# Optimization experiments

Hardware: AMD Instinct MI355X
Metric: run time of the kernel (lower is better)

Reference implementation:

```python
import jax, jax.numpy as jnp
import numpy as np

# Dims: R radiance slots (patch,direction), E sparse transfer entries, T echogram samples, P patches
R, E, T, P = 4096, 131072, 1536, 256
NUM_BOUNCES = 12
FSM_GAMMA = 1e-3
SAMPLE_RATE = 16000.0


def setup_inputs() -> dict:
    key = jax.random.key(0)
    ks = jax.random.split(key, 10)
    initial_radiance = jax.random.normal(ks[0], (R, T), dtype=jnp.float32)
    # basis scaled so per-bounce operator row-sums < 1 (stable recursion, as real kernels are)
    basis = jax.random.uniform(ks[1], (2, E), dtype=jnp.float32) * (1.0 / 64.0)
    absorption = jax.random.uniform(ks[2], (P,), dtype=jnp.float32)
    scattering = jax.random.uniform(ks[3], (P,), dtype=jnp.float32)
    detection_weights = jax.random.uniform(ks[4], (R,), dtype=jnp.float32)
    row = jax.random.randint(ks[5], (E,), 0, R)
    col = jax.random.randint(ks[6], (E,), 0, R)
    reflector_ids = jax.random.randint(ks[7], (E,), 0, P)
    delay_samples = jax.random.randint(ks[8], (E,), 0, 512)
    detection_delay = jax.random.randint(ks[9], (R,), 0, 256)
    return dict(initial_radiance=initial_radiance, basis=basis, absorption=absorption,
                scattering=scattering, detection_weights=detection_weights,
                row=row, col=col, reflector_ids=reflector_ids,
                delay_samples=delay_samples, detection_delay=detection_delay)


def reference(initial_radiance, basis, absorption, scattering, detection_weights,
              row, col, reflector_ids, delay_samples, detection_delay):
    Rn, Tn = initial_radiance.shape
    F = Tn // 2 + 1
    # FSM damping window exp(log(gamma) * t), undone after the frequency-domain loop
    t = jnp.arange(Tn, dtype=jnp.float32) / SAMPLE_RATE
    fsm_window = jnp.exp(np.float32(np.log(FSM_GAMMA)) * t)  # [T]
    # compose_kernel: per-edge reflection kernel from per-patch absorption/scattering
    a = absorption[reflector_ids]
    s = scattering[reflector_ids]
    kern = (1.0 - a) * (s * basis[0] + (1.0 - s) * basis[1])  # [E]
    # per-edge integer-delay as frequency-domain phase ramp
    f = jnp.arange(F, dtype=jnp.float32)
    edge_phase = jnp.exp(-2j * np.pi * (delay_samples.astype(jnp.float32)[:, None] * f[None, :] / Tn))
    kc = kern.astype(jnp.complex64)[:, None] * edge_phase.astype(jnp.complex64)  # [E, F]
    # injected radiance in frequency domain (damped)
    Xf = jnp.fft.rfft(initial_radiance * fsm_window[None, :], axis=-1).astype(jnp.complex64)  # [R, F]

    def bounce(carry, _):
        cur, tot = carry
        msg = kc * cur[col]                                    # gather + sparse multiply [E, F]
        nxt = jax.ops.segment_sum(msg, row, num_segments=Rn)   # scatter-add -> [R, F]
        return (nxt, tot + nxt), None

    (_, total), _ = jax.lax.scan(bounce, (Xf, Xf), None, length=NUM_BOUNCES)
    # detection: per-radiance delayed weighted sum at the receiver
    det_phase = jnp.exp(-2j * np.pi * (detection_delay.astype(jnp.float32)[:, None] * f[None, :] / Tn))
    echo_f = jnp.einsum('r,rf->f', detection_weights.astype(jnp.complex64),
                        det_phase.astype(jnp.complex64) * total)
    echogram = jnp.fft.irfft(echo_f, n=Tn) / fsm_window  # FSM correction
    return echogram
```

## Files before the change

kernel.cpp:

```cpp
#include <hip/hip_runtime.h>
#include <hip/hip_bf16.h>
#include <hip/hip_fp16.h>

#define RN 4096
#define EN 131072
#define TN 1536
#define T2 768
#define SP 1040
#define PADP 257
#define PN 256
#define NBOUNCE 12
#define NCHUNK 4
#define CP 192
#define LOG_GAMMA -6.90775528f
#define INV_SR (1.0f / 16000.0f)

#define rfl(x) __builtin_amdgcn_readfirstlane(x)


__global__ void hist_kernel(const int* __restrict__ row, const int* __restrict__ col,
                            int* __restrict__ cnt2) {
    int e = blockIdx.x * blockDim.x + threadIdx.x;
    if (e < EN) atomicAdd(&cnt2[row[e] * 2 + (col[e] >> 11)], 1);
}

__global__ void scan_kernel(const int* __restrict__ cnt2, int* __restrict__ off,
                            int* __restrict__ cursor2, int* __restrict__ ntot) {
    __shared__ int part[1024];
    int tid = threadIdx.x;
    int l0 = cnt2[(tid * 4 + 0) * 2], h0 = cnt2[(tid * 4 + 0) * 2 + 1];
    int l1 = cnt2[(tid * 4 + 1) * 2], h1 = cnt2[(tid * 4 + 1) * 2 + 1];
    int l2 = cnt2[(tid * 4 + 2) * 2], h2 = cnt2[(tid * 4 + 2) * 2 + 1];
    int l3 = cnt2[(tid * 4 + 3) * 2], h3 = cnt2[(tid * 4 + 3) * 2 + 1];
    int n0 = l0 + h0, n1 = l1 + h1, n2 = l2 + h2, n3 = l3 + h3;
    int p0 = (n0 + 1) & ~1, p1 = (n1 + 1) & ~1, p2 = (n2 + 1) & ~1, p3 = (n3 + 1) & ~1;
    part[tid] = p0 + p1 + p2 + p3;
    __syncthreads();
    for (int ofs = 1; ofs < 1024; ofs <<= 1) {
        int x = (tid >= ofs) ? part[tid - ofs] : 0;
        __syncthreads();
        part[tid] += x;
        __syncthreads();
    }
    int excl = (tid == 0) ? 0 : part[tid - 1];
    int o0 = excl, o1 = o0 + p0, o2 = o1 + p1, o3 = o2 + p2;
    int r0 = tid * 4;
    off[r0 + 0] = o0; cursor2[(r0 + 0) * 2] = o0; cursor2[(r0 + 0) * 2 + 1] = o0 + l0; ntot[r0 + 0] = n0;
    off[r0 + 1] = o1; cursor2[(r0 + 1) * 2] = o1; cursor2[(r0 + 1) * 2 + 1] = o1 + l1; ntot[r0 + 1] = n1;
    off[r0 + 2] = o2; cursor2[(r0 + 2) * 2] = o2; cursor2[(r0 + 2) * 2 + 1] = o2 + l2; ntot[r0 + 2] = n2;
    off[r0 + 3] = o3; cursor2[(r0 + 3) * 2] = o3; cursor2[(r0 + 3) * 2 + 1] = o3 + l3; ntot[r0 + 3] = n3;
    if (tid == 1023) off[RN] = o3 + p3;
}

__global__ void scatter_kernel(const int* __restrict__ row, const int* __restrict__ col,
                               const int* __restrict__ rid, const int* __restrict__ delay,
                               const float* __restrict__ basis,
                               const float* __restrict__ absorption,
                               const float* __restrict__ scattering,
                               int* __restrict__ cursor2, int2* __restrict__ mdarr) {
    int e = blockIdx.x * blockDim.x + threadIdx.x;
    if (e >= EN) return;
    int p = rid[e];
    float a = absorption[p];
    float s = scattering[p];
    float k = (1.0f - a) * (s * basis[e] + (1.0f - s) * basis[EN + e]);
    int d = delay[e];
    int c = col[e];
    int dpair = (d + 1) >> 1;
    int o = ((c * SP + PADP - dpair) << 2) | (d & 1);
    int pos = atomicAdd(&cursor2[row[e] * 2 + (c >> 11)], 1);
    mdarr[pos] = make_int2(o, __float_as_int(k));
}

__global__ void padfill_kernel(const int* __restrict__ off, const int* __restrict__ ntot,
                               int2* __restrict__ mdarr) {
    int r = blockIdx.x * 256 + threadIdx.x;
    if (r < RN) {
        int n = ntot[r];
        if (n & 1) mdarr[off[r] + n] = make_int2(PADP << 2, 0);
    }
    if (r < 8) mdarr[off[RN] + r] = make_int2(PADP << 2, 0);
}


__global__ __launch_bounds__(256) void init_kernel(const float* __restrict__ x,
                                                   __half* __restrict__ cur) {
    int r = blockIdx.x;
    int tid = threadIdx.x;
    const float* xr = x + r * TN;
    uint* curp = (uint*)cur + (size_t)r * SP;
#pragma unroll
    for (int kk = 0; kk < 3; ++kk) {
        int q = tid + kk * 256;
        int t = q * 2;
        float wa = __expf(LOG_GAMMA * (float)t * INV_SR);
        float wb = __expf(LOG_GAMMA * (float)(t + 1) * INV_SR);
        __half2 h = __float22half2_rn(make_float2(xr[t] * wa, xr[t + 1] * wb));
        uint u = *(uint*)&h;
        curp[PADP + q] = u;
        if (q >= 511) curp[q - 511] = u;
    }
}


#define ISSUE(W, mo)                                                   \
    {                                                                  \
        const uint* rp_ = (const uint*)(curb + (size_t)((mo) & ~1u));  \
        W = *(const uint4*)(rp_ + pb);                                 \
    }

#define CONSUME(W, mo, kb)                                             \
    {                                                                  \
        float k_ = __uint_as_float((uint)(kb));                        \
        uint v0_, v1_, v2_;                                            \
        if ((mo) & 1u) {                                               \
            v0_ = __builtin_amdgcn_alignbit(W.y, W.x, 16);             \
            v1_ = __builtin_amdgcn_alignbit(W.z, W.y, 16);             \
            v2_ = __builtin_amdgcn_alignbit(W.w, W.z, 16);             \
        } else { v0_ = W.x; v1_ = W.y; v2_ = W.z; }                    \
        __half2 h0_ = *(__half2*)&v0_;                                 \
        __half2 h1_ = *(__half2*)&v1_;                                 \
        __half2 h2_ = *(__half2*)&v2_;                                 \
        a0 = fmaf(k_, __half2float(h0_.x), a0);                        \
        a1 = fmaf(k_, __half2float(h0_.y), a1);                        \
        a2 = fmaf(k_, __half2float(h1_.x), a2);                        \
        a3 = fmaf(k_, __half2float(h1_.y), a3);                        \
        a4 = fmaf(k_, __half2float(h2_.x), a4);                        \
        a5 = fmaf(k_, __half2float(h2_.y), a5);                        \
    }

__global__ __launch_bounds__(128, 8) void bounce_kernel(
        const __half* __restrict__ cur, __half* __restrict__ nxt,
        const int* __restrict__ offp, const int* __restrict__ ntot,
        const int2* __restrict__ mdarr) {
    int bid = blockIdx.x;
    int rg = bid >> 2;
    int chunk = bid & 3;
    int wave = threadIdx.x >> 6;
    int lane = threadIdx.x & 63;
    int r = rg * 2 + wave;
    int c0 = chunk * CP;
    int pb = c0 + lane * 3;
    int e0 = rfl(offp[r]);
    int n  = rfl(ntot[r]);
    float a0 = 0.f, a1 = 0.f, a2 = 0.f, a3 = 0.f, a4 = 0.f, a5 = 0.f;
    const char* curb = (const char*)cur;

    if (n > 0) {
        int e1p = e0 + ((n + 1) & ~1);
        uint4 md01 = *(const uint4*)(mdarr + e0);
        uint moA = (uint)rfl((int)md01.x), kbA = (uint)rfl((int)md01.y);
        uint moB = (uint)rfl((int)md01.z), kbB = (uint)rfl((int)md01.w);
        uint4 WA, WB;
        ISSUE(WA, moA);
        ISSUE(WB, moB);
        for (int j = e0 + 2; j < e1p; j += 2) {
            uint4 mdn = *(const uint4*)(mdarr + j);
            uint moC = (uint)rfl((int)mdn.x), kbC = (uint)rfl((int)mdn.y);
            uint moD = (uint)rfl((int)mdn.z), kbD = (uint)rfl((int)mdn.w);
            CONSUME(WA, moA, kbA); ISSUE(WA, moC);
            CONSUME(WB, moB, kbB); ISSUE(WB, moD);
            moA = moC; kbA = kbC; moB = moD; kbB = kbD;
        }
        CONSUME(WA, moA, kbA);
        CONSUME(WB, moB, kbB);
    }

    __half2 h0 = __float22half2_rn(make_float2(a0, a1));
    __half2 h1 = __float22half2_rn(make_float2(a2, a3));
    __half2 h2 = __float22half2_rn(make_float2(a4, a5));
    uint u0 = *(uint*)&h0, u1 = *(uint*)&h1, u2 = *(uint*)&h2;
    uint* nxtp = (uint*)nxt + (size_t)r * SP;
    nxtp[PADP + pb]     = u0;
    nxtp[PADP + pb + 1] = u1;
    nxtp[PADP + pb + 2] = u2;
    if (pb + 2 >= 511) {
        if (pb     >= 511) nxtp[pb - 511] = u0;
        if (pb + 1 >= 511) nxtp[pb - 510] = u1;
        nxtp[pb - 509] = u2;
    }
}


__global__ __launch_bounds__(128) void detect_kernel(
        const __half* __restrict__ buf, const float* __restrict__ w,
        const int* __restrict__ dd, float* __restrict__ det) {
    int cx = blockIdx.x;
    int r0 = blockIdx.y * 16;
    int tid = threadIdx.x;
    int tb = cx * 384 + tid;
    float acc0 = 0.f, acc1 = 0.f, acc2 = 0.f;
#pragma unroll 4
    for (int rr = 0; rr < 16; ++rr) {
        int r = r0 + rr;
        int d = dd[r];
        float wr = w[r];
        const __half* bufr = buf + (size_t)r * (SP * 2);
        int s0 = tb - d;           if (s0 < 0) s0 += TN;
        int s1 = tb + 128 - d;     if (s1 < 0) s1 += TN;
        int s2 = tb + 256 - d;     if (s2 < 0) s2 += TN;
        acc0 = fmaf(wr, __half2float(bufr[(PADP + (s0 >> 1)) * 2 + (s0 & 1)]), acc0);
        acc1 = fmaf(wr, __half2float(bufr[(PADP + (s1 >> 1)) * 2 + (s1 & 1)]), acc1);
        acc2 = fmaf(wr, __half2float(bufr[(PADP + (s2 >> 1)) * 2 + (s2 & 1)]), acc2);
    }
    atomicAdd(&det[tb], acc0);
    atomicAdd(&det[tb + 128], acc1);
    atomicAdd(&det[tb + 256], acc2);
}

__global__ void final_kernel(const float* __restrict__ det, float* __restrict__ out) {
    int t = blockIdx.x * 256 + threadIdx.x;
    if (t < TN) out[t] = det[t] * __expf(-LOG_GAMMA * (float)t * INV_SR);
}


extern "C" void kernel_launch(void* const* d_in, const int* in_sizes, int n_in,
                              void* d_out, int out_size, void* d_ws, size_t ws_size,
                              hipStream_t stream) {
    const float* init_rad   = (const float*)d_in[0];
    const float* basis      = (const float*)d_in[1];
    const float* absorption = (const float*)d_in[2];
    const float* scattering = (const float*)d_in[3];
    const float* det_w      = (const float*)d_in[4];
    const int*   row        = (const int*)d_in[5];
    const int*   col        = (const int*)d_in[6];
    const int*   rid        = (const int*)d_in[7];
    const int*   delay      = (const int*)d_in[8];
    const int*   det_delay  = (const int*)d_in[9];
    float* out = (float*)d_out;

    char* ws = (char*)d_ws;
    size_t o = 0;
    auto alloc = [&](size_t bytes) {
        void* p = ws + o;
        o = (o + bytes + 255) & ~(size_t)255;
        return p;
    };
    int*    cnt2    = (int*)alloc(RN * 2 * 4);
    int*    off     = (int*)alloc((RN + 1) * 4);
    int*    cursor2 = (int*)alloc(RN * 2 * 4);
    int*    ntot    = (int*)alloc(RN * 4);
    int2*   mdarr   = (int2*)alloc((size_t)(EN + RN + 8) * 8);
    __half* bufA    = (__half*)alloc((size_t)RN * SP * 4);
    __half* bufB    = (__half*)alloc((size_t)RN * SP * 4);
    float*  det     = (float*)alloc(TN * 4);

    hipMemsetAsync(cnt2, 0, RN * 2 * 4, stream);
    hipMemsetAsync(det, 0, TN * 4, stream);

    hist_kernel<<<EN / 256, 256, 0, stream>>>(row, col, cnt2);
    scan_kernel<<<1, 1024, 0, stream>>>(cnt2, off, cursor2, ntot);
    scatter_kernel<<<EN / 256, 256, 0, stream>>>(row, col, rid, delay, basis,
                                                 absorption, scattering, cursor2, mdarr);
    padfill_kernel<<<RN / 256, 256, 0, stream>>>(off, ntot, mdarr);
    init_kernel<<<RN, 256, 0, stream>>>(init_rad, bufA);

    dim3 dgrid(NCHUNK, RN / 16);
    detect_kernel<<<dgrid, 128, 0, stream>>>(bufA, det_w, det_delay, det);

    __half* cur = bufA;
    __half* nxt = bufB;
    for (int b = 0; b < NBOUNCE; ++b) {
        bounce_kernel<<<(RN / 2) * NCHUNK, 128, 0, stream>>>(cur, nxt, off, ntot, mdarr);
        detect_kernel<<<dgrid, 128, 0, stream>>>(nxt, det_w, det_delay, det);
        __half* tmp = cur; cur = nxt; nxt = tmp;
    }

    final_kernel<<<TN / 256, 256, 0, stream>>>(det, out);
}
```

Measured before the change: 627.4 us.

## Process four rows per wave in low/high column phases for gather locality

Each bounce wave now handles four rows spread across the matrix and sweeps all their low-column edges before the high-column edges, so gathers hit the same half of the source buffer together and cache reuse should improve. Separate low/high counters replace the interleaved histogram, and the even-padding of edge lists plus the padfill kernel are removed. The edge loop becomes a one-deep prefetch pipeline, occupancy hints drop to 4 blocks, and output stores become nontemporal. The trade is less memory-level parallelism per wave and more registers in exchange for locality.

```diff
diff --git a/kernel.cpp b/kernel.cpp
--- a/kernel.cpp
+++ b/kernel.cpp
@@ -19,22 +19,25 @@
 
 
 __global__ void hist_kernel(const int* __restrict__ row, const int* __restrict__ col,
-                            int* __restrict__ cnt2) {
+                            int* __restrict__ cntL, int* __restrict__ cntH) {
     int e = blockIdx.x * blockDim.x + threadIdx.x;
-    if (e < EN) atomicAdd(&cnt2[row[e] * 2 + (col[e] >> 11)], 1);
-}
-
-__global__ void scan_kernel(const int* __restrict__ cnt2, int* __restrict__ off,
-                            int* __restrict__ cursor2, int* __restrict__ ntot) {
+    if (e >= EN) return;
+    int r = row[e];
+    if (col[e] < 2048) atomicAdd(&cntL[r], 1);
+    else               atomicAdd(&cntH[r], 1);
+}
+
+__global__ void scan_kernel(const int* __restrict__ cntL, const int* __restrict__ cntH,
+                            int* __restrict__ off, int* __restrict__ curL,
+                            int* __restrict__ curH) {
     __shared__ int part[1024];
     int tid = threadIdx.x;
-    int l0 = cnt2[(tid * 4 + 0) * 2], h0 = cnt2[(tid * 4 + 0) * 2 + 1];
-    int l1 = cnt2[(tid * 4 + 1) * 2], h1 = cnt2[(tid * 4 + 1) * 2 + 1];
-    int l2 = cnt2[(tid * 4 + 2) * 2], h2 = cnt2[(tid * 4 + 2) * 2 + 1];
-    int l3 = cnt2[(tid * 4 + 3) * 2], h3 = cnt2[(tid * 4 + 3) * 2 + 1];
+    int l0 = cntL[tid * 4 + 0], h0 = cntH[tid * 4 + 0];
+    int l1 = cntL[tid * 4 + 1], h1 = cntH[tid * 4 + 1];
+    int l2 = cntL[tid * 4 + 2], h2 = cntH[tid * 4 + 2];
+    int l3 = cntL[tid * 4 + 3], h3 = cntH[tid * 4 + 3];
     int n0 = l0 + h0, n1 = l1 + h1, n2 = l2 + h2, n3 = l3 + h3;
-    int p0 = (n0 + 1) & ~1, p1 = (n1 + 1) & ~1, p2 = (n2 + 1) & ~1, p3 = (n3 + 1) & ~1;
-    part[tid] = p0 + p1 + p2 + p3;
+    part[tid] = n0 + n1 + n2 + n3;
     __syncthreads();
     for (int ofs = 1; ofs < 1024; ofs <<= 1) {
         int x = (tid >= ofs) ? part[tid - ofs] : 0;
@@ -43,13 +46,13 @@
         __syncthreads();
     }
     int excl = (tid == 0) ? 0 : part[tid - 1];
-    int o0 = excl, o1 = o0 + p0, o2 = o1 + p1, o3 = o2 + p2;
+    int o0 = excl, o1 = o0 + n0, o2 = o1 + n1, o3 = o2 + n2;
     int r0 = tid * 4;
-    off[r0 + 0] = o0; cursor2[(r0 + 0) * 2] = o0; cursor2[(r0 + 0) * 2 + 1] = o0 + l0; ntot[r0 + 0] = n0;
-    off[r0 + 1] = o1; cursor2[(r0 + 1) * 2] = o1; cursor2[(r0 + 1) * 2 + 1] = o1 + l1; ntot[r0 + 1] = n1;
-    off[r0 + 2] = o2; cursor2[(r0 + 2) * 2] = o2; cursor2[(r0 + 2) * 2 + 1] = o2 + l2; ntot[r0 + 2] = n2;
-    off[r0 + 3] = o3; cursor2[(r0 + 3) * 2] = o3; cursor2[(r0 + 3) * 2 + 1] = o3 + l3; ntot[r0 + 3] = n3;
-    if (tid == 1023) off[RN] = o3 + p3;
+    off[r0 + 0] = o0; curL[r0 + 0] = o0; curH[r0 + 0] = o0 + l0;
+    off[r0 + 1] = o1; curL[r0 + 1] = o1; curH[r0 + 1] = o1 + l1;
+    off[r0 + 2] = o2; curL[r0 + 2] = o2; curH[r0 + 2] = o2 + l2;
+    off[r0 + 3] = o3; curL[r0 + 3] = o3; curH[r0 + 3] = o3 + l3;
+    if (tid == 1023) off[RN] = o3 + n3;
 }
 
 __global__ void scatter_kernel(const int* __restrict__ row, const int* __restrict__ col,
@@ -57,7 +60,8 @@
                                const float* __restrict__ basis,
                                const float* __restrict__ absorption,
                                const float* __restrict__ scattering,
-                               int* __restrict__ cursor2, int2* __restrict__ mdarr) {
+                               int* __restrict__ curL, int* __restrict__ curH,
+                               int2* __restrict__ mdarr) {
     int e = blockIdx.x * blockDim.x + threadIdx.x;
     if (e >= EN) return;
     int p = rid[e];
@@ -68,18 +72,9 @@
     int c = col[e];
     int dpair = (d + 1) >> 1;
     int o = ((c * SP + PADP - dpair) << 2) | (d & 1);
-    int pos = atomicAdd(&cursor2[row[e] * 2 + (c >> 11)], 1);
+    int r = row[e];
+    int pos = (c < 2048) ? atomicAdd(&curL[r], 1) : atomicAdd(&curH[r], 1);
     mdarr[pos] = make_int2(o, __float_as_int(k));
-}
-
-__global__ void padfill_kernel(const int* __restrict__ off, const int* __restrict__ ntot,
-                               int2* __restrict__ mdarr) {
-    int r = blockIdx.x * 256 + threadIdx.x;
-    if (r < RN) {
-        int n = ntot[r];
-        if (n & 1) mdarr[off[r] + n] = make_int2(PADP << 2, 0);
-    }
-    if (r < 8) mdarr[off[RN] + r] = make_int2(PADP << 2, 0);
 }
 
 
@@ -109,7 +104,7 @@
         W = *(const uint4*)(rp_ + pb);                                 \
     }
 
-#define CONSUME(W, mo, kb)                                             \
+#define CONSUME(W, mo, kb, ACC)                                        \
     {                                                                  \
         float k_ = __uint_as_float((uint)(kb));                        \
         uint v0_, v1_, v2_;                                            \
@@ -121,63 +116,74 @@
         __half2 h0_ = *(__half2*)&v0_;                                 \
         __half2 h1_ = *(__half2*)&v1_;                                 \
         __half2 h2_ = *(__half2*)&v2_;                                 \
-        a0 = fmaf(k_, __half2float(h0_.x), a0);                        \
-        a1 = fmaf(k_, __half2float(h0_.y), a1);                        \
-        a2 = fmaf(k_, __half2float(h1_.x), a2);                        \
-        a3 = fmaf(k_, __half2float(h1_.y), a3);                        \
-        a4 = fmaf(k_, __half2float(h2_.x), a4);                        \
-        a5 = fmaf(k_, __half2float(h2_.y), a5);                        \
-    }
-
-__global__ __launch_bounds__(128, 8) void bounce_kernel(
+        ACC[0] = fmaf(k_, __half2float(h0_.x), ACC[0]);                \
+        ACC[1] = fmaf(k_, __half2float(h0_.y), ACC[1]);                \
+        ACC[2] = fmaf(k_, __half2float(h1_.x), ACC[2]);                \
+        ACC[3] = fmaf(k_, __half2float(h1_.y), ACC[3]);                \
+        ACC[4] = fmaf(k_, __half2float(h2_.x), ACC[4]);                \
+        ACC[5] = fmaf(k_, __half2float(h2_.y), ACC[5]);                \
+    }
+
+#define SEGMENT(S0, S1, ACC)                                           \
+    if ((S1) > (S0)) {                                                 \
+        int2 md = mdarr[S0];                                           \
+        uint mo = (uint)rfl(md.x), kb = (uint)rfl(md.y);               \
+        uint4 W; ISSUE(W, mo);                                         \
+        for (int j = (S0) + 1; j < (S1); ++j) {                        \
+            int2 mdn = mdarr[j];                                       \
+            uint moN = (uint)rfl(mdn.x), kbN = (uint)rfl(mdn.y);       \
+            uint4 WN; ISSUE(WN, moN);                                  \
+            CONSUME(W, mo, kb, ACC);                                   \
+            W = WN; mo = moN; kb = kbN;                                \
+        }                                                              \
+        CONSUME(W, mo, kb, ACC);                                       \
+    }
+
+__global__ __launch_bounds__(128, 4) void bounce_kernel(
         const __half* __restrict__ cur, __half* __restrict__ nxt,
-        const int* __restrict__ offp, const int* __restrict__ ntot,
+        const int* __restrict__ offp, const int* __restrict__ cntL,
         const int2* __restrict__ mdarr) {
     int bid = blockIdx.x;
-    int rg = bid >> 2;
     int chunk = bid & 3;
+    int rgrp = bid >> 2;
     int wave = threadIdx.x >> 6;
     int lane = threadIdx.x & 63;
-    int r = rg * 2 + wave;
     int c0 = chunk * CP;
     int pb = c0 + lane * 3;
-    int e0 = rfl(offp[r]);
-    int n  = rfl(ntot[r]);
-    float a0 = 0.f, a1 = 0.f, a2 = 0.f, a3 = 0.f, a4 = 0.f, a5 = 0.f;
     const char* curb = (const char*)cur;
 
-    if (n > 0) {
-        int e1p = e0 + ((n + 1) & ~1);
-        uint4 md01 = *(const uint4*)(mdarr + e0);
-        uint moA = (uint)rfl((int)md01.x), kbA = (uint)rfl((int)md01.y);
-        uint moB = (uint)rfl((int)md01.z), kbB = (uint)rfl((int)md01.w);
-        uint4 WA, WB;
-        ISSUE(WA, moA);
-        ISSUE(WB, moB);
-        for (int j = e0 + 2; j < e1p; j += 2) {
-            uint4 mdn = *(const uint4*)(mdarr + j);
-            uint moC = (uint)rfl((int)mdn.x), kbC = (uint)rfl((int)mdn.y);
-            uint moD = (uint)rfl((int)mdn.z), kbD = (uint)rfl((int)mdn.w);
-            CONSUME(WA, moA, kbA); ISSUE(WA, moC);
-            CONSUME(WB, moB, kbB); ISSUE(WB, moD);
-            moA = moC; kbA = kbC; moB = moD; kbB = kbD;
+    float acc[4][6] = {};
+
+#pragma unroll
+    for (int ph = 0; ph < 2; ++ph) {
+#pragma unroll
+        for (int L = 0; L < 4; ++L) {
+            int r = rgrp * 2 + wave + 1024 * L;
+            int o0 = rfl(offp[r]);
+            int o1 = rfl(offp[r + 1]);
+            int lo = rfl(cntL[r]);
+            int s0 = ph ? (o0 + lo) : o0;
+            int s1 = ph ? o1 : (o0 + lo);
+            SEGMENT(s0, s1, acc[L]);
         }
-        CONSUME(WA, moA, kbA);
-        CONSUME(WB, moB, kbB);
-    }
-
-    __half2 h0 = __float22half2_rn(make_float2(a0, a1));
-    __half2 h1 = __float22half2_rn(make_float2(a2, a3));
-    __half2 h2 = __float22half2_rn(make_float2(a4, a5));
-    uint u0 = *(uint*)&h0, u1 = *(uint*)&h1, u2 = *(uint*)&h2;
-    uint* nxtp = (uint*)nxt + (size_t)r * SP;
-    nxtp[PADP + pb]     = u0;
-    nxtp[PADP + pb + 1] = u1;
-    nxtp[PADP + pb + 2] = u2;
-    if (pb + 2 >= 511) {
-        if (pb     >= 511) nxtp[pb - 511] = u0;
-        if (pb + 1 >= 511) nxtp[pb - 510] = u1;
-        nxtp[pb - 509] = u2;
+    }
+
+#pragma unroll
+    for (int L = 0; L < 4; ++L) {
+        int r = rgrp * 2 + wave + 1024 * L;
+        __half2 h0 = __float22half2_rn(make_float2(acc[L][0], acc[L][1]));
+        __half2 h1 = __float22half2_rn(make_float2(acc[L][2], acc[L][3]));
+        __half2 h2 = __float22half2_rn(make_float2(acc[L][4], acc[L][5]));
+        uint u0 = *(uint*)&h0, u1 = *(uint*)&h1, u2 = *(uint*)&h2;
+        uint* nxtp = (uint*)nxt + (size_t)r * SP;
+        __builtin_nontemporal_store(u0, nxtp + PADP + pb);
+        __builtin_nontemporal_store(u1, nxtp + PADP + pb + 1);
+        __builtin_nontemporal_store(u2, nxtp + PADP + pb + 2);
+        if (pb + 2 >= 511) {
+            if (pb     >= 511) __builtin_nontemporal_store(u0, nxtp + pb - 511);
+            if (pb + 1 >= 511) __builtin_nontemporal_store(u1, nxtp + pb - 510);
+            __builtin_nontemporal_store(u2, nxtp + pb - 509);
+        }
     }
 }
 
@@ -236,23 +242,25 @@
         o = (o + bytes + 255) & ~(size_t)255;
         return p;
     };
-    int*    cnt2    = (int*)alloc(RN * 2 * 4);
-    int*    off     = (int*)alloc((RN + 1) * 4);
-    int*    cursor2 = (int*)alloc(RN * 2 * 4);
-    int*    ntot    = (int*)alloc(RN * 4);
-    int2*   mdarr   = (int2*)alloc((size_t)(EN + RN + 8) * 8);
-    __half* bufA    = (__half*)alloc((size_t)RN * SP * 4);
-    __half* bufB    = (__half*)alloc((size_t)RN * SP * 4);
-    float*  det     = (float*)alloc(TN * 4);
-
-    hipMemsetAsync(cnt2, 0, RN * 2 * 4, stream);
+    int*    cntL   = (int*)alloc(RN * 4);
+    int*    cntH   = (int*)alloc(RN * 4);
+    int*    curL   = (int*)alloc(RN * 4);
+    int*    curH   = (int*)alloc(RN * 4);
+    int*    off    = (int*)alloc((RN + 1) * 4);
+    int2*   mdarr  = (int2*)alloc((size_t)EN * 8);
+    __half* bufA   = (__half*)alloc((size_t)RN * SP * 4);
+    __half* bufB   = (__half*)alloc((size_t)RN * SP * 4);
+    float*  det    = (float*)alloc(TN * 4);
+
+    hipMemsetAsync(cntL, 0, RN * 4, stream);
+    hipMemsetAsync(cntH, 0, RN * 4, stream);
     hipMemsetAsync(det, 0, TN * 4, stream);
 
-    hist_kernel<<<EN / 256, 256, 0, stream>>>(row, col, cnt2);
-    scan_kernel<<<1, 1024, 0, stream>>>(cnt2, off, cursor2, ntot);
+    hist_kernel<<<EN / 256, 256, 0, stream>>>(row, col, cntL, cntH);
+    scan_kernel<<<1, 1024, 0, stream>>>(cntL, cntH, off, curL, curH);
     scatter_kernel<<<EN / 256, 256, 0, stream>>>(row, col, rid, delay, basis,
-                                                 absorption, scattering, cursor2, mdarr);
-    padfill_kernel<<<RN / 256, 256, 0, stream>>>(off, ntot, mdarr);
+                                                 absorption, scattering, curL, curH,
+                                                 mdarr);
     init_kernel<<<RN, 256, 0, stream>>>(init_rad, bufA);
 
     dim3 dgrid(NCHUNK, RN / 16);
@@ -261,7 +269,7 @@
     __half* cur = bufA;
     __half* nxt = bufB;
     for (int b = 0; b < NBOUNCE; ++b) {
-        bounce_kernel<<<(RN / 2) * NCHUNK, 128, 0, stream>>>(cur, nxt, off, ntot, mdarr);
+        bounce_kernel<<<2048, 128, 0, stream>>>(cur, nxt, off, cntL, mdarr);
         detect_kernel<<<dgrid, 128, 0, stream>>>(nxt, det_w, det_delay, det);
         __half* tmp = cur; cur = nxt; nxt = tmp;
     }
```

Result: slower. 941.4 us (+50.1%).

## Store radiance buffers as fp8 with byte-granular delay gathers

Applied to the files above, without the earlier changes.

The radiance state moves from fp16 pairs to fp8 (e4m3) bytes, halving the gather traffic in the bounce kernel and in detection. Edge offsets become plain byte offsets with a byte alignment shift, and output rows are repacked through LDS for aligned 8-byte stores. The initial detection pass now reads the fp32 input directly so the injected term keeps full precision. The risk is a large accuracy loss, since fp8 carries only 3 mantissa bits and a narrow range across 12 compounding bounces, and the output may fail tolerance.

```diff
diff --git a/kernel.cpp b/kernel.cpp
--- a/kernel.cpp
+++ b/kernel.cpp
@@ -5,17 +5,18 @@
 #define RN 4096
 #define EN 131072
 #define TN 1536
-#define T2 768
-#define SP 1040
-#define PADP 257
+#define SPB 2064
+#define PADB 512
 #define PN 256
 #define NBOUNCE 12
 #define NCHUNK 4
-#define CP 192
+#define CPB 384
 #define LOG_GAMMA -6.90775528f
 #define INV_SR (1.0f / 16000.0f)
 
 #define rfl(x) __builtin_amdgcn_readfirstlane(x)
+typedef float v2f __attribute__((ext_vector_type(2)));
+typedef unsigned char uchar;
 
 
 __global__ void hist_kernel(const int* __restrict__ row, const int* __restrict__ col,
@@ -64,10 +65,8 @@
     float a = absorption[p];
     float s = scattering[p];
     float k = (1.0f - a) * (s * basis[e] + (1.0f - s) * basis[EN + e]);
-    int d = delay[e];
     int c = col[e];
-    int dpair = (d + 1) >> 1;
-    int o = ((c * SP + PADP - dpair) << 2) | (d & 1);
+    int o = c * SPB + PADB - delay[e];
     int pos = atomicAdd(&cursor2[row[e] * 2 + (c >> 11)], 1);
     mdarr[pos] = make_int2(o, __float_as_int(k));
 }
@@ -77,60 +76,60 @@
     int r = blockIdx.x * 256 + threadIdx.x;
     if (r < RN) {
         int n = ntot[r];
-        if (n & 1) mdarr[off[r] + n] = make_int2(PADP << 2, 0);
-    }
-    if (r < 8) mdarr[off[RN] + r] = make_int2(PADP << 2, 0);
-}
-
-
-__global__ __launch_bounds__(256) void init_kernel(const float* __restrict__ x,
-                                                   __half* __restrict__ cur) {
+        if (n & 1) mdarr[off[r] + n] = make_int2(PADB, 0);
+    }
+    if (r < 8) mdarr[off[RN] + r] = make_int2(PADB, 0);
+}
+
+
+__global__ __launch_bounds__(128) void init_kernel(const float* __restrict__ x,
+                                                   uchar* __restrict__ cur) {
     int r = blockIdx.x;
     int tid = threadIdx.x;
     const float* xr = x + r * TN;
-    uint* curp = (uint*)cur + (size_t)r * SP;
+    uchar* rowb = cur + (size_t)r * SPB;
 #pragma unroll
     for (int kk = 0; kk < 3; ++kk) {
-        int q = tid + kk * 256;
-        int t = q * 2;
-        float wa = __expf(LOG_GAMMA * (float)t * INV_SR);
-        float wb = __expf(LOG_GAMMA * (float)(t + 1) * INV_SR);
-        __half2 h = __float22half2_rn(make_float2(xr[t] * wa, xr[t + 1] * wb));
-        uint u = *(uint*)&h;
-        curp[PADP + q] = u;
-        if (q >= 511) curp[q - 511] = u;
+        int j = tid + kk * 128;
+        int t = j * 4;
+        float f0 = xr[t + 0] * __expf(LOG_GAMMA * (float)(t + 0) * INV_SR);
+        float f1 = xr[t + 1] * __expf(LOG_GAMMA * (float)(t + 1) * INV_SR);
+        float f2 = xr[t + 2] * __expf(LOG_GAMMA * (float)(t + 2) * INV_SR);
+        float f3 = xr[t + 3] * __expf(LOG_GAMMA * (float)(t + 3) * INV_SR);
+        uint u = (uint)__builtin_amdgcn_cvt_pk_fp8_f32(f0, f1, 0, false);
+        u = (uint)__builtin_amdgcn_cvt_pk_fp8_f32(f2, f3, (int)u, true);
+        *(uint*)(rowb + PADB + t) = u;
+        if (t >= 1024) *(uint*)(rowb + t - 1024) = u;
     }
 }
 
 
 #define ISSUE(W, mo)                                                   \
     {                                                                  \
-        const uint* rp_ = (const uint*)(curb + (size_t)((mo) & ~1u));  \
-        W = *(const uint4*)(rp_ + pb);                                 \
+        uint ab_ = (uint)(mo) + (uint)pbB;                             \
+        W = *(const uint4*)(curb + (ab_ & ~3u));                       \
     }
 
 #define CONSUME(W, mo, kb)                                             \
     {                                                                  \
         float k_ = __uint_as_float((uint)(kb));                        \
-        uint v0_, v1_, v2_;                                            \
-        if ((mo) & 1u) {                                               \
-            v0_ = __builtin_amdgcn_alignbit(W.y, W.x, 16);             \
-            v1_ = __builtin_amdgcn_alignbit(W.z, W.y, 16);             \
-            v2_ = __builtin_amdgcn_alignbit(W.w, W.z, 16);             \
-        } else { v0_ = W.x; v1_ = W.y; v2_ = W.z; }                    \
-        __half2 h0_ = *(__half2*)&v0_;                                 \
-        __half2 h1_ = *(__half2*)&v1_;                                 \
-        __half2 h2_ = *(__half2*)&v2_;                                 \
-        a0 = fmaf(k_, __half2float(h0_.x), a0);                        \
-        a1 = fmaf(k_, __half2float(h0_.y), a1);                        \
-        a2 = fmaf(k_, __half2float(h1_.x), a2);                        \
-        a3 = fmaf(k_, __half2float(h1_.y), a3);                        \
-        a4 = fmaf(k_, __half2float(h2_.x), a4);                        \
-        a5 = fmaf(k_, __half2float(h2_.y), a5);                        \
+        uint ab_ = (uint)(mo) + (uint)pbB;                             \
+        uint sh_ = ab_ & 3u;                                           \
+        uint b0_ = __builtin_amdgcn_alignbyte(W.y, W.x, sh_);          \
+        uint b1_ = __builtin_amdgcn_alignbyte(W.z, W.y, sh_);          \
+        v2f f01_ = __builtin_amdgcn_cvt_pk_f32_fp8((int)b0_, false);   \
+        v2f f23_ = __builtin_amdgcn_cvt_pk_f32_fp8((int)b0_, true);    \
+        v2f f45_ = __builtin_amdgcn_cvt_pk_f32_fp8((int)b1_, false);   \
+        a0 = fmaf(k_, f01_.x, a0);                                     \
+        a1 = fmaf(k_, f01_.y, a1);                                     \
+        a2 = fmaf(k_, f23_.x, a2);                                     \
+        a3 = fmaf(k_, f23_.y, a3);                                     \
+        a4 = fmaf(k_, f45_.x, a4);                                     \
+        a5 = fmaf(k_, f45_.y, a5);                                     \
     }
 
 __global__ __launch_bounds__(128, 8) void bounce_kernel(
-        const __half* __restrict__ cur, __half* __restrict__ nxt,
+        const uchar* __restrict__ cur, uchar* __restrict__ nxt,
         const int* __restrict__ offp, const int* __restrict__ ntot,
         const int2* __restrict__ mdarr) {
     int bid = blockIdx.x;
@@ -139,12 +138,11 @@
     int wave = threadIdx.x >> 6;
     int lane = threadIdx.x & 63;
     int r = rg * 2 + wave;
-    int c0 = chunk * CP;
-    int pb = c0 + lane * 3;
+    int pbB = chunk * CPB + lane * 6;
     int e0 = rfl(offp[r]);
     int n  = rfl(ntot[r]);
     float a0 = 0.f, a1 = 0.f, a2 = 0.f, a3 = 0.f, a4 = 0.f, a5 = 0.f;
-    const char* curb = (const char*)cur;
+    const uchar* curb = cur;
 
     if (n > 0) {
         int e1p = e0 + ((n + 1) & ~1);
@@ -166,24 +164,28 @@
         CONSUME(WB, moB, kbB);
     }
 
-    __half2 h0 = __float22half2_rn(make_float2(a0, a1));
-    __half2 h1 = __float22half2_rn(make_float2(a2, a3));
-    __half2 h2 = __float22half2_rn(make_float2(a4, a5));
-    uint u0 = *(uint*)&h0, u1 = *(uint*)&h1, u2 = *(uint*)&h2;
-    uint* nxtp = (uint*)nxt + (size_t)r * SP;
-    nxtp[PADP + pb]     = u0;
-    nxtp[PADP + pb + 1] = u1;
-    nxtp[PADP + pb + 2] = u2;
-    if (pb + 2 >= 511) {
-        if (pb     >= 511) nxtp[pb - 511] = u0;
-        if (pb + 1 >= 511) nxtp[pb - 510] = u1;
-        nxtp[pb - 509] = u2;
-    }
-}
-
-
-__global__ __launch_bounds__(128) void detect_kernel(
-        const __half* __restrict__ buf, const float* __restrict__ w,
+    __shared__ uint ldsw[256];
+    uchar* lds = (uchar*)ldsw;
+    uint lo = (uint)__builtin_amdgcn_cvt_pk_fp8_f32(a0, a1, 0, false);
+    lo = (uint)__builtin_amdgcn_cvt_pk_fp8_f32(a2, a3, (int)lo, true);
+    uint hi = (uint)__builtin_amdgcn_cvt_pk_fp8_f32(a4, a5, 0, false);
+    int lb = wave * 512 + lane * 6;
+    *(ushort*)&lds[lb]     = (ushort)(lo & 0xffffu);
+    *(ushort*)&lds[lb + 2] = (ushort)(lo >> 16);
+    *(ushort*)&lds[lb + 4] = (ushort)(hi & 0xffffu);
+    __syncthreads();
+    if (lane < 48) {
+        uint2 u = *(uint2*)&lds[wave * 512 + lane * 8];
+        int sbase = chunk * CPB + lane * 8;
+        uchar* rowb = nxt + (size_t)r * SPB;
+        *(uint2*)(rowb + PADB + sbase) = u;
+        if (sbase >= 1024) *(uint2*)(rowb + sbase - 1024) = u;
+    }
+}
+
+
+__global__ __launch_bounds__(128) void detect0_kernel(
+        const float* __restrict__ x, const float* __restrict__ w,
         const int* __restrict__ dd, float* __restrict__ det) {
     int cx = blockIdx.x;
     int r0 = blockIdx.y * 16;
@@ -195,13 +197,39 @@
         int r = r0 + rr;
         int d = dd[r];
         float wr = w[r];
-        const __half* bufr = buf + (size_t)r * (SP * 2);
+        const float* xr = x + (size_t)r * TN;
         int s0 = tb - d;           if (s0 < 0) s0 += TN;
         int s1 = tb + 128 - d;     if (s1 < 0) s1 += TN;
         int s2 = tb + 256 - d;     if (s2 < 0) s2 += TN;
-        acc0 = fmaf(wr, __half2float(bufr[(PADP + (s0 >> 1)) * 2 + (s0 & 1)]), acc0);
-        acc1 = fmaf(wr, __half2float(bufr[(PADP + (s1 >> 1)) * 2 + (s1 & 1)]), acc1);
-        acc2 = fmaf(wr, __half2float(bufr[(PADP + (s2 >> 1)) * 2 + (s2 & 1)]), acc2);
+        acc0 = fmaf(wr * __expf(LOG_GAMMA * (float)s0 * INV_SR), xr[s0], acc0);
+        acc1 = fmaf(wr * __expf(LOG_GAMMA * (float)s1 * INV_SR), xr[s1], acc1);
+        acc2 = fmaf(wr * __expf(LOG_GAMMA * (float)s2 * INV_SR), xr[s2], acc2);
+    }
+    atomicAdd(&det[tb], acc0);
+    atomicAdd(&det[tb + 128], acc1);
+    atomicAdd(&det[tb + 256], acc2);
+}
+
+__global__ __launch_bounds__(128) void detect_kernel(
+        const uchar* __restrict__ buf, const float* __restrict__ w,
+        const int* __restrict__ dd, float* __restrict__ det) {
+    int cx = blockIdx.x;
+    int r0 = blockIdx.y * 16;
+    int tid = threadIdx.x;
+    int tb = cx * 384 + tid;
+    float acc0 = 0.f, acc1 = 0.f, acc2 = 0.f;
+#pragma unroll 4
+    for (int rr = 0; rr < 16; ++rr) {
+        int r = r0 + rr;
+        int d = dd[r];
+        float wr = w[r];
+        const uchar* bufr = buf + (size_t)r * SPB;
+        v2f v0 = __builtin_amdgcn_cvt_pk_f32_fp8((int)(uint)bufr[PADB + tb - d], false);
+        v2f v1 = __builtin_amdgcn_cvt_pk_f32_fp8((int)(uint)bufr[PADB + tb + 128 - d], false);
+        v2f v2 = __builtin_amdgcn_cvt_pk_f32_fp8((int)(uint)bufr[PADB + tb + 256 - d], false);
+        acc0 = fmaf(wr, v0.x, acc0);
+        acc1 = fmaf(wr, v1.x, acc1);
+        acc2 = fmaf(wr, v2.x, acc2);
     }
     atomicAdd(&det[tb], acc0);
     atomicAdd(&det[tb + 128], acc1);
@@ -236,14 +264,14 @@
         o = (o + bytes + 255) & ~(size_t)255;
         return p;
     };
-    int*    cnt2    = (int*)alloc(RN * 2 * 4);
-    int*    off     = (int*)alloc((RN + 1) * 4);
-    int*    cursor2 = (int*)alloc(RN * 2 * 4);
-    int*    ntot    = (int*)alloc(RN * 4);
-    int2*   mdarr   = (int2*)alloc((size_t)(EN + RN + 8) * 8);
-    __half* bufA    = (__half*)alloc((size_t)RN * SP * 4);
-    __half* bufB    = (__half*)alloc((size_t)RN * SP * 4);
-    float*  det     = (float*)alloc(TN * 4);
+    int*   cnt2    = (int*)alloc(RN * 2 * 4);
+    int*   cursor2 = (int*)alloc(RN * 2 * 4);
+    int*   ntot    = (int*)alloc(RN * 4);
+    int*   off     = (int*)alloc((RN + 1) * 4);
+    int2*  mdarr   = (int2*)alloc((size_t)(EN + RN + 8) * 8);
+    uchar* bufA    = (uchar*)alloc((size_t)RN * SPB);
+    uchar* bufB    = (uchar*)alloc((size_t)RN * SPB);
+    float* det     = (float*)alloc(TN * 4);
 
     hipMemsetAsync(cnt2, 0, RN * 2 * 4, stream);
     hipMemsetAsync(det, 0, TN * 4, stream);
@@ -253,17 +281,17 @@
     scatter_kernel<<<EN / 256, 256, 0, stream>>>(row, col, rid, delay, basis,
                                                  absorption, scattering, cursor2, mdarr);
     padfill_kernel<<<RN / 256, 256, 0, stream>>>(off, ntot, mdarr);
-    init_kernel<<<RN, 256, 0, stream>>>(init_rad, bufA);
+    init_kernel<<<RN, 128, 0, stream>>>(init_rad, bufA);
 
     dim3 dgrid(NCHUNK, RN / 16);
-    detect_kernel<<<dgrid, 128, 0, stream>>>(bufA, det_w, det_delay, det);
-
-    __half* cur = bufA;
-    __half* nxt = bufB;
+    detect0_kernel<<<dgrid, 128, 0, stream>>>(init_rad, det_w, det_delay, det);
+
+    uchar* cur = bufA;
+    uchar* nxt = bufB;
     for (int b = 0; b < NBOUNCE; ++b) {
         bounce_kernel<<<(RN / 2) * NCHUNK, 128, 0, stream>>>(cur, nxt, off, ntot, mdarr);
         detect_kernel<<<dgrid, 128, 0, stream>>>(nxt, det_w, det_delay, det);
-        __half* tmp = cur; cur = nxt; nxt = tmp;
+        uchar* tmp = cur; cur = nxt; nxt = tmp;
     }
 
     final_kernel<<<TN / 256, 256, 0, stream>>>(det, out);
```

Result: faster. 530.0 us (-15.5%).
